# Performance work log

Measured on AMD Instinct MI355X. Metric: run time of the kernel, lower is better.

Reference implementation:

```python
import jax, jax.numpy as jnp
import numpy as np

# SofthebbArgs constants (rate, adaptive=True, p, dot_uw=False, temp)
RATE = 1e-3
TEMP = 1.0
P = 0.5


def negate_non_maximal(t):
    # keep the per-row max entry, negate all others
    idx = jnp.argmax(t, axis=-1)                      # [B]
    mask = idx[:, None] == jnp.arange(t.shape[-1])    # [B, OUT]
    return jnp.where(mask, t, -t)


def setup_inputs() -> dict:
    key = jax.random.key(0)
    k1, k2 = jax.random.split(key, 2)
    B, IN, OUT = 8192, 1024, 1024
    x = jax.random.normal(k1, (B, IN), dtype=jnp.float32)
    # xavier_normal_ with gain=1: std = sqrt(2/(fan_in+fan_out))
    W = jax.random.normal(k2, (OUT, IN), dtype=jnp.float32) * (2.0 / (IN + OUT)) ** 0.5
    b = jnp.zeros((OUT,), dtype=jnp.float32)
    return {"x": x, "W": W, "b": b}


def reference(x, W, b):
    # --- HebbianLinear.forward (act = Identity) ---
    u = x @ W.T + b                                   # [B, OUT]
    y = u
    # --- softhebb: y = softmax(y / temp), then _hebb with dot_uw=False ---
    ysm = jax.nn.softmax(y / TEMP, axis=1)
    yn = negate_non_maximal(ysm)                      # [B, OUT]
    Bn = x.shape[0]
    # _hebb materializes dw[b,o,i] = yn[b,o]*(x[b,i] - u[b,o]*W[o,i]) then means over b.
    # Algebraically fused (no [B,OUT,IN] intermediate):
    #   step[o,i] = (yn^T x)[o,i]/B - mean_b(yn[b,o]*u[b,o]) * W[o,i]
    step = (yn.T @ x) / Bn - jnp.mean(yn * u, axis=0)[:, None] * W  # [OUT, IN]
    # adaptive per-row rate: rate * |1 - ||W_row||_2|^p
    diff = jnp.abs(1.0 - jnp.linalg.norm(W, axis=1))  # [OUT]
    rate = RATE * diff ** P
    return rate[:, None] * step                       # [OUT, IN]
```

## Files before the change

kernel.cpp:

```cpp
#include <hip/hip_runtime.h>

#define BATCH 8192
#define INF_  1024
#define OUTF  1024
#define INV_B (1.0f/8192.0f)
#define RATE_C 1e-3f
#define SPLITZ 16

typedef __bf16 bf16x8 __attribute__((ext_vector_type(8)));
typedef float  f32x4  __attribute__((ext_vector_type(4)));
typedef const __attribute__((address_space(1))) unsigned int* gas_t;
typedef __attribute__((address_space(3))) unsigned int* las_t;

static __device__ __forceinline__ unsigned short f2bf(float f) {
  unsigned int u = __float_as_uint(f);
  u += 0x7fffu + ((u >> 16) & 1u);
  return (unsigned short)(u >> 16);
}
static __device__ __forceinline__ float bf2f(unsigned short h) {
  return __uint_as_float(((unsigned int)h) << 16);
}

__global__ __launch_bounds__(256) void k_convert(
    const float* __restrict__ x, unsigned short* __restrict__ xb,
    unsigned short* __restrict__ xT, const float* __restrict__ W,
    unsigned short* __restrict__ Wb, float* __restrict__ rate) {
  const int t = threadIdx.x;
  if (blockIdx.x >= 2048) {
    __shared__ float red[256];
    const int o = blockIdx.x - 2048;
    float4 v = *(const float4*)&W[(size_t)o * INF_ + t * 4];
    ushort4 h;
    h.x = f2bf(v.x); h.y = f2bf(v.y); h.z = f2bf(v.z); h.w = f2bf(v.w);
    *(ushort4*)&Wb[(size_t)o * INF_ + t * 4] = h;
    red[t] = v.x * v.x + v.y * v.y + v.z * v.z + v.w * v.w;
    __syncthreads();
    for (int s = 128; s > 0; s >>= 1) {
      if (t < s) red[t] += red[t + s];
      __syncthreads();
    }
    if (t == 0) {
      float nrm = sqrtf(red[0]);
      rate[o] = RATE_C * sqrtf(fabsf(1.0f - nrm));
    }
    return;
  }
  __shared__ unsigned int t32[64][33];
  const int bx = blockIdx.x & 15;
  const int by = blockIdx.x >> 4;
  const int r0 = by * 64;
  const int c0 = bx * 64;
  const int m = t & 15;
  const int q = t >> 4;
#pragma unroll
  for (int p = 0; p < 2; ++p) {
    const int r2 = p * 16 + q;
    const int b  = r0 + 2 * r2;
    float4 v0 = *(const float4*)&x[(size_t)b * INF_ + c0 + 4 * m];
    float4 v1 = *(const float4*)&x[(size_t)(b + 1) * INF_ + c0 + 4 * m];
    ushort4 h0, h1;
    h0.x = f2bf(v0.x); h0.y = f2bf(v0.y); h0.z = f2bf(v0.z); h0.w = f2bf(v0.w);
    h1.x = f2bf(v1.x); h1.y = f2bf(v1.y); h1.z = f2bf(v1.z); h1.w = f2bf(v1.w);
    *(ushort4*)&xb[(size_t)b * INF_ + c0 + 4 * m] = h0;
    *(ushort4*)&xb[(size_t)(b + 1) * INF_ + c0 + 4 * m] = h1;
    t32[4 * m + 0][r2] = (unsigned int)h0.x | ((unsigned int)h1.x << 16);
    t32[4 * m + 1][r2] = (unsigned int)h0.y | ((unsigned int)h1.y << 16);
    t32[4 * m + 2][r2] = (unsigned int)h0.z | ((unsigned int)h1.z << 16);
    t32[4 * m + 3][r2] = (unsigned int)h0.w | ((unsigned int)h1.w << 16);
  }
  __syncthreads();
  const int c  = t >> 2;
  const int sg = t & 3;
  unsigned int vb[8];
#pragma unroll
  for (int k = 0; k < 8; ++k) vb[k] = t32[c][sg * 8 + k];
  unsigned short* dst = &xT[(size_t)(c0 + c) * BATCH + r0 + sg * 16];
  *(uint4*)&dst[0] = make_uint4(vb[0], vb[1], vb[2], vb[3]);
  *(uint4*)&dst[8] = make_uint4(vb[4], vb[5], vb[6], vb[7]);
}

__global__ __launch_bounds__(256, 3) void k_gemm(
    const unsigned short* __restrict__ A, const unsigned short* __restrict__ B,
    int lda, int ldb, int kChunk, void* __restrict__ C, int ldc,
    const float* __restrict__ bias, int mode) {
  __shared__ unsigned short As[128 * 64];
  __shared__ unsigned short Bs[128 * 64];
  const int t  = threadIdx.x;
  const int id = blockIdx.x;
  int bx, by, bz;
  if (mode == 0) {
    by = (id & 7) | ((id >> 6) << 3);
    bx = (id >> 3) & 7;
    bz = 0;
  } else {
    bz = ((id & 7) << 1) | ((id >> 3) & 1);
    by = (id >> 4) & 7;
    bx = id >> 7;
  }
  const int m0   = by * 128;
  const int n0   = bx * 128;
  const int k0   = bz * kChunk;
  const int lane = t & 63;
  const int wave = t >> 6;
  const int sr   = lane >> 3;
  const int scx  = ((lane & 7) ^ sr) * 8;
  const int wm   = (wave >> 1) * 64;
  const int wn   = (wave & 1) * 64;
  const int fm   = lane & 15;
  const int fk   = (lane >> 4) * 8;

  f32x4 acc[4][4] = {};

  const int ldsRow0 = wave * 8;
  const size_t gArow = (size_t)(m0 + ldsRow0 + sr) * lda + scx;
  const size_t gBrow = (size_t)(n0 + ldsRow0 + sr) * ldb + scx;

  for (int ks = 0; ks < kChunk; ks += 64) {
    const int k = k0 + ks;
#pragma unroll
    for (int j = 0; j < 4; ++j) {
      __builtin_amdgcn_global_load_lds(
          (gas_t)&A[gArow + (size_t)j * 32 * lda + k],
          (las_t)&As[(ldsRow0 + j * 32) * 64], 16, 0, 0);
      __builtin_amdgcn_global_load_lds(
          (gas_t)&B[gBrow + (size_t)j * 32 * ldb + k],
          (las_t)&Bs[(ldsRow0 + j * 32) * 64], 16, 0, 0);
    }
    __syncthreads();
#pragma unroll
    for (int kk = 0; kk < 64; kk += 32) {
      bf16x8 af[4], bf[4];
      const int swz = ((((kk + fk) >> 3) ^ (fm & 7)) << 3);
#pragma unroll
      for (int i = 0; i < 4; ++i)
        af[i] = *(const bf16x8*)&As[(wm + i * 16 + fm) * 64 + swz];
#pragma unroll
      for (int i = 0; i < 4; ++i)
        bf[i] = *(const bf16x8*)&Bs[(wn + i * 16 + fm) * 64 + swz];
#pragma unroll
      for (int mt = 0; mt < 4; ++mt)
#pragma unroll
        for (int nt = 0; nt < 4; ++nt)
          acc[mt][nt] = __builtin_amdgcn_mfma_f32_16x16x32_bf16(
              af[mt], bf[nt], acc[mt][nt], 0, 0, 0);
    }
    __syncthreads();
  }

  const int er = (lane >> 4) * 4;
  if (mode == 0) {
    unsigned short* Cb = (unsigned short*)C;
#pragma unroll
    for (int nt = 0; nt < 4; ++nt) {
      const int n  = n0 + wn + nt * 16 + fm;
      const float bv = bias[n];
#pragma unroll
      for (int mt = 0; mt < 4; ++mt) {
        const int mb = m0 + wm + mt * 16 + er;
#pragma unroll
        for (int r = 0; r < 4; ++r)
          Cb[(size_t)(mb + r) * ldc + n] = f2bf(acc[mt][nt][r] + bv);
      }
    }
  } else {
    unsigned short* Cp = (unsigned short*)C + (size_t)bz * (1024u * 1024u);
#pragma unroll
    for (int nt = 0; nt < 4; ++nt) {
      const int n = n0 + wn + nt * 16 + fm;
#pragma unroll
      for (int mt = 0; mt < 4; ++mt) {
        const int mb = m0 + wm + mt * 16 + er;
#pragma unroll
        for (int r = 0; r < 4; ++r)
          Cp[(size_t)(mb + r) * ldc + n] = f2bf(acc[mt][nt][r]);
      }
    }
  }
}

__global__ __launch_bounds__(256, 2) void k_softhebb(
    const unsigned short* __restrict__ ub, const float* __restrict__ x,
    const float* __restrict__ W, unsigned short* __restrict__ ynT,
    float* __restrict__ s_part) {
  __shared__ unsigned short tile[16][1032];
  __shared__ int cands[4][32];
  __shared__ int cnt[4];
  const int t     = threadIdx.x;
  const int lane  = t & 63;
  const int wave  = t >> 6;
  const int b0    = blockIdx.x * 16;
  const int oBase = lane * 16;

  float sacc[16];
#pragma unroll
  for (int j = 0; j < 16; ++j) sacc[j] = 0.0f;

  for (int rw = 0; rw < 4; ++rw) {
    const int r = wave * 4 + rw;
    const int b = b0 + r;
    float a[16];
    {
      uint4 q0 = *(const uint4*)&ub[(size_t)b * OUTF + oBase];
      uint4 q1 = *(const uint4*)&ub[(size_t)b * OUTF + oBase + 8];
      const unsigned int* qa = (const unsigned int*)&q0;
      const unsigned int* qb = (const unsigned int*)&q1;
#pragma unroll
      for (int c = 0; c < 4; ++c) {
        a[2 * c]     = __uint_as_float(qa[c] << 16);
        a[2 * c + 1] = __uint_as_float(qa[c] & 0xffff0000u);
        a[8 + 2 * c]     = __uint_as_float(qb[c] << 16);
        a[8 + 2 * c + 1] = __uint_as_float(qb[c] & 0xffff0000u);
      }
    }
    float mv = a[0]; int mi = oBase;
#pragma unroll
    for (int j = 1; j < 16; ++j)
      if (a[j] > mv) { mv = a[j]; mi = oBase + j; }
#pragma unroll
    for (int off = 1; off < 64; off <<= 1) {
      float ov = __shfl_xor(mv, off);
      int   oi = __shfl_xor(mi, off);
      if (ov > mv || (ov == mv && oi < mi)) { mv = ov; mi = oi; }
    }
    const float M = mv;
    float se = 0.0f;
#pragma unroll
    for (int j = 0; j < 16; ++j) se += __expf(a[j] - M);
#pragma unroll
    for (int off = 1; off < 64; off <<= 1) se += __shfl_xor(se, off);

    const float thr = M - 0.10f;
    unsigned int cflags = 0;
    int ccount = 0;
#pragma unroll
    for (int j = 0; j < 16; ++j)
      if (a[j] >= thr) { cflags |= (1u << j); ++ccount; }
    int tot = ccount;
#pragma unroll
    for (int off = 1; off < 64; off <<= 1) tot += __shfl_xor(tot, off);

    int best = mi;
    if (tot > 1) {
      if (lane == 0) cnt[wave] = 0;
      for (int j = 0; j < 16; ++j)
        if (cflags & (1u << j)) {
          int p = atomicAdd(&cnt[wave], 1);
          if (p < 32) cands[wave][p] = oBase + j;
        }
      int nc = cnt[wave]; if (nc > 32) nc = 32;
      float xr[16];
      const float* xp = &x[(size_t)b * INF_ + oBase];
#pragma unroll
      for (int j = 0; j < 16; j += 4) {
        float4 v = *(const float4*)&xp[j];
        xr[j] = v.x; xr[j + 1] = v.y; xr[j + 2] = v.z; xr[j + 3] = v.w;
      }
      float bv = -3.4e38f; int bi = 0x7fffffff;
      for (int c = 0; c < nc; ++c) {
        const int o = cands[wave][c];
        const float* wp = &W[(size_t)o * INF_ + oBase];
        float d = 0.0f;
#pragma unroll
        for (int j = 0; j < 16; j += 4) {
          float4 v = *(const float4*)&wp[j];
          d += xr[j] * v.x + xr[j + 1] * v.y + xr[j + 2] * v.z +
               xr[j + 3] * v.w;
        }
#pragma unroll
        for (int off = 1; off < 64; off <<= 1) d += __shfl_xor(d, off);
        if (d > bv || (d == bv && o < bi)) { bv = d; bi = o; }
      }
      best = bi;
    }

    const float inv = 1.0f / se;
    uint4 pka, pkb;
    unsigned short* p0v = (unsigned short*)&pka;
    unsigned short* p1v = (unsigned short*)&pkb;
#pragma unroll
    for (int j = 0; j < 16; ++j) {
      float e  = __expf(a[j] - M) * inv;
      float yn = (oBase + j == best) ? e : -e;
      sacc[j] += yn * a[j];
      unsigned short hv = f2bf(yn);
      if (j < 8) p0v[j] = hv; else p1v[j - 8] = hv;
    }
    const int c0 = 2 * lane, c1 = 2 * lane + 1;
    const int sp0 = c0 ^ ((c0 >> 1) & 7);
    const int sp1 = c1 ^ ((c1 >> 1) & 7);
    *(uint4*)&tile[r][sp0 * 8] = pka;
    *(uint4*)&tile[r][sp1 * 8] = pkb;
  }

  {
    float* sp = &s_part[(size_t)(blockIdx.x * 4 + wave) * OUTF + oBase];
#pragma unroll
    for (int j = 0; j < 16; j += 4)
      *(float4*)&sp[j] = make_float4(sacc[j], sacc[j + 1], sacc[j + 2],
                                     sacc[j + 3]);
  }
  __syncthreads();

#pragma unroll
  for (int i = 0; i < 4; ++i) {
    const int o  = t + 256 * i;
    const int c  = o >> 3;
    const int sp = c ^ ((c >> 1) & 7);
    const int off = o & 7;
    uint4 v0, v1;
    unsigned short* va = (unsigned short*)&v0;
    unsigned short* vb = (unsigned short*)&v1;
#pragma unroll
    for (int r = 0; r < 8; ++r)  va[r] = tile[r][sp * 8 + off];
#pragma unroll
    for (int r = 0; r < 8; ++r)  vb[r] = tile[r + 8][sp * 8 + off];
    unsigned short* dst = &ynT[(size_t)o * BATCH + b0];
    *(uint4*)&dst[0] = v0;
    *(uint4*)&dst[8] = v1;
  }
}

__global__ __launch_bounds__(256) void k_final(
    const unsigned short* __restrict__ Cp, const float* __restrict__ W,
    const float* __restrict__ s_part, const float* __restrict__ rate,
    float* __restrict__ out) {
  __shared__ float sred[256];
  const int t  = threadIdx.x;
  const int id = blockIdx.x;
  const int o  = ((id & 7) << 7) | (id >> 3);
  float sa = 0.0f;
  for (int k = t; k < 2048; k += 256) sa += s_part[(size_t)k * OUTF + o];
  sred[t] = sa;
  __syncthreads();
  for (int s2 = 128; s2 > 0; s2 >>= 1) {
    if (t < s2) sred[t] += sred[t + s2];
    __syncthreads();
  }
  const float sb = sred[0] * INV_B;
  const float rt = rate[o];
  const int i0 = t * 4;
  float cx = 0, cy = 0, cz = 0, cw = 0;
#pragma unroll
  for (int z = 0; z < SPLITZ; ++z) {
    ushort4 h = *(const ushort4*)&Cp[(size_t)z * (1024u * 1024u) +
                                     (size_t)o * INF_ + i0];
    cx += bf2f(h.x); cy += bf2f(h.y); cz += bf2f(h.z); cw += bf2f(h.w);
  }
  float4 w = *(const float4*)&W[(size_t)o * INF_ + i0];
  float4 r;
  r.x = rt * (cx * INV_B - sb * w.x);
  r.y = rt * (cy * INV_B - sb * w.y);
  r.z = rt * (cz * INV_B - sb * w.z);
  r.w = rt * (cw * INV_B - sb * w.w);
  *(float4*)&out[(size_t)o * INF_ + i0] = r;
}

extern "C" void kernel_launch(void* const* d_in, const int* in_sizes, int n_in,
                              void* d_out, int out_size, void* d_ws, size_t ws_size,
                              hipStream_t stream) {
  const float* x    = (const float*)d_in[0];
  const float* W    = (const float*)d_in[1];
  const float* bias = (const float*)d_in[2];
  float* out = (float*)d_out;
  char* ws = (char*)d_ws;

  unsigned short* ub    = (unsigned short*)(ws + 0);
  unsigned short* xb    = (unsigned short*)(ws + 16777216);
  unsigned short* xT    = (unsigned short*)(ws + 33554432);
  unsigned short* ynT   = (unsigned short*)(ws + 50331648);
  unsigned short* Wb    = (unsigned short*)(ws + 67108864);
  float*          rate  = (float*)(ws + 69206016);
  float*          spart = (float*)(ws + 69210112);

  k_convert<<<dim3(3072), 256, 0, stream>>>(x, xb, xT, W, Wb, rate);
  k_gemm<<<dim3(512), 256, 0, stream>>>(xb, Wb, 1024, 1024, 1024,
                                        ub, 1024, bias, 0);
  k_softhebb<<<dim3(512), 256, 0, stream>>>(ub, x, W, ynT, spart);
  k_gemm<<<dim3(1024), 256, 0, stream>>>(ynT, xT, 8192, 8192, 512,
                                         ws, 1024, nullptr, 1);
  k_final<<<dim3(1024), 256, 0, stream>>>((const unsigned short*)ws, W, spart,
                                          rate, out);
}
```

Before: 164.1 us.

## Process 32 rows per softhebb block and reduce row partials in shared memory

Each softhebb block now handles 32 batch rows instead of 16, so the transposed ynT stores become 64-byte contiguous runs per output column. The four per-wave partial sums of yn*u are reduced in shared memory before being written, which cuts the s_part buffer from 2048 to 256 rows. That in turn shrinks the strided reduction loop in k_final to a single load per thread. In exchange the grid has half as many blocks, shared memory per block doubles, and two extra barriers are added.

```diff
diff --git a/kernel.cpp b/kernel.cpp
--- a/kernel.cpp
+++ b/kernel.cpp
@@ -182,21 +182,21 @@
     const unsigned short* __restrict__ ub, const float* __restrict__ x,
     const float* __restrict__ W, unsigned short* __restrict__ ynT,
     float* __restrict__ s_part) {
-  __shared__ unsigned short tile[16][1032];
+  __shared__ unsigned short tile[32][1032];
   __shared__ int cands[4][32];
   __shared__ int cnt[4];
   const int t     = threadIdx.x;
   const int lane  = t & 63;
   const int wave  = t >> 6;
-  const int b0    = blockIdx.x * 16;
+  const int b0    = blockIdx.x * 32;
   const int oBase = lane * 16;
 
   float sacc[16];
 #pragma unroll
   for (int j = 0; j < 16; ++j) sacc[j] = 0.0f;
 
-  for (int rw = 0; rw < 4; ++rw) {
-    const int r = wave * 4 + rw;
+  for (int rw = 0; rw < 8; ++rw) {
+    const int r = wave * 8 + rw;
     const int b = b0 + r;
     float a[16];
     {
@@ -291,32 +291,39 @@
     *(uint4*)&tile[r][sp0 * 8] = pka;
     *(uint4*)&tile[r][sp1 * 8] = pkb;
   }
-
+  __syncthreads();
+
+#pragma unroll
+  for (int i = 0; i < 4; ++i) {
+    const int o   = t + 256 * i;
+    const int c   = o >> 3;
+    const int sp  = c ^ ((c >> 1) & 7);
+    const int off = o & 7;
+    unsigned short buf[32];
+#pragma unroll
+    for (int r = 0; r < 32; ++r) buf[r] = tile[r][sp * 8 + off];
+    unsigned short* dst = &ynT[(size_t)o * BATCH + b0];
+    *(uint4*)&dst[0]  = *(const uint4*)&buf[0];
+    *(uint4*)&dst[8]  = *(const uint4*)&buf[8];
+    *(uint4*)&dst[16] = *(const uint4*)&buf[16];
+    *(uint4*)&dst[24] = *(const uint4*)&buf[24];
+  }
+  __syncthreads();
+
+  float* fred = (float*)tile;
+#pragma unroll
+  for (int j = 0; j < 16; j += 4)
+    *(f32x4*)&fred[wave * 1024 + oBase + j] =
+        *(const f32x4*)&sacc[j];
+  __syncthreads();
   {
-    float* sp = &s_part[(size_t)(blockIdx.x * 4 + wave) * OUTF + oBase];
-#pragma unroll
-    for (int j = 0; j < 16; j += 4)
-      *(float4*)&sp[j] = make_float4(sacc[j], sacc[j + 1], sacc[j + 2],
-                                     sacc[j + 3]);
-  }
-  __syncthreads();
-
-#pragma unroll
-  for (int i = 0; i < 4; ++i) {
-    const int o  = t + 256 * i;
-    const int c  = o >> 3;
-    const int sp = c ^ ((c >> 1) & 7);
-    const int off = o & 7;
-    uint4 v0, v1;
-    unsigned short* va = (unsigned short*)&v0;
-    unsigned short* vb = (unsigned short*)&v1;
-#pragma unroll
-    for (int r = 0; r < 8; ++r)  va[r] = tile[r][sp * 8 + off];
-#pragma unroll
-    for (int r = 0; r < 8; ++r)  vb[r] = tile[r + 8][sp * 8 + off];
-    unsigned short* dst = &ynT[(size_t)o * BATCH + b0];
-    *(uint4*)&dst[0] = v0;
-    *(uint4*)&dst[8] = v1;
+    const int o4 = t * 4;
+    f32x4 s0 = *(const f32x4*)&fred[o4];
+    f32x4 s1 = *(const f32x4*)&fred[1024 + o4];
+    f32x4 s2 = *(const f32x4*)&fred[2048 + o4];
+    f32x4 s3 = *(const f32x4*)&fred[3072 + o4];
+    f32x4 sum = s0 + s1 + s2 + s3;
+    *(f32x4*)&s_part[(size_t)blockIdx.x * OUTF + o4] = sum;
   }
 }
 
@@ -328,9 +335,7 @@
   const int t  = threadIdx.x;
   const int id = blockIdx.x;
   const int o  = ((id & 7) << 7) | (id >> 3);
-  float sa = 0.0f;
-  for (int k = t; k < 2048; k += 256) sa += s_part[(size_t)k * OUTF + o];
-  sred[t] = sa;
+  sred[t] = s_part[(size_t)t * OUTF + o];
   __syncthreads();
   for (int s2 = 128; s2 > 0; s2 >>= 1) {
     if (t < s2) sred[t] += sred[t + s2];
@@ -375,7 +380,7 @@
   k_convert<<<dim3(3072), 256, 0, stream>>>(x, xb, xT, W, Wb, rate);
   k_gemm<<<dim3(512), 256, 0, stream>>>(xb, Wb, 1024, 1024, 1024,
                                         ub, 1024, bias, 0);
-  k_softhebb<<<dim3(512), 256, 0, stream>>>(ub, x, W, ynT, spart);
+  k_softhebb<<<dim3(256), 256, 0, stream>>>(ub, x, W, ynT, spart);
   k_gemm<<<dim3(1024), 256, 0, stream>>>(ynT, xT, 8192, 8192, 512,
                                          ws, 1024, nullptr, 1);
   k_final<<<dim3(1024), 256, 0, stream>>>((const unsigned short*)ws, W, spart,
```

Result: no change. 164.1 us (+0.0%).
